# Optimization experiments

Hardware: AMD Instinct MI355X
Metric: run time of the kernel (lower is better)

Reference implementation:

```python
import jax, jax.numpy as jnp
import numpy as np

EPS = 1e-5  # BatchNorm eps
N_NODES, N_EDGES, F = 100000, 600000, 128


def setup_inputs() -> dict:
    key = jax.random.key(0)
    ks = jax.random.split(key, 16)
    inp = {
        "node_representations": jax.random.normal(ks[0], (N_NODES, F), jnp.float32),
        "edges": jax.random.randint(ks[1], (2, N_EDGES), 0, N_NODES, jnp.int64 if jax.config.jax_enable_x64 else jnp.int32),
        "edge_weights": jax.random.uniform(ks[2], (N_EDGES,), jnp.float32),
        # preprocess FFN: BatchNorm1d(F) [eval mode] + Linear(F, F) + GELU
        "pre_bn_gamma": jax.random.normal(ks[3], (F,), jnp.float32) * 0.1 + 1.0,
        "pre_bn_beta": jax.random.normal(ks[4], (F,), jnp.float32) * 0.1,
        "pre_bn_mean": jax.random.normal(ks[5], (F,), jnp.float32) * 0.1,
        "pre_bn_var": jax.random.uniform(ks[6], (F,), jnp.float32) * 0.5 + 0.5,
        "pre_w": jax.random.normal(ks[7], (F, F), jnp.float32) / np.sqrt(F),
        "pre_b": jnp.zeros((F,), jnp.float32),
        # update FFN: BatchNorm1d(2F) [eval mode] + Linear(2F, F) + GELU
        "upd_bn_gamma": jax.random.normal(ks[8], (2 * F,), jnp.float32) * 0.1 + 1.0,
        "upd_bn_beta": jax.random.normal(ks[9], (2 * F,), jnp.float32) * 0.1,
        "upd_bn_mean": jax.random.normal(ks[10], (2 * F,), jnp.float32) * 0.1,
        "upd_bn_var": jax.random.uniform(ks[11], (2 * F,), jnp.float32) * 0.5 + 0.5,
        "upd_w": jax.random.normal(ks[12], (2 * F, F), jnp.float32) / np.sqrt(2 * F),
        "upd_b": jnp.zeros((F,), jnp.float32),
    }
    return inp


def _bn_eval(x, gamma, beta, mean, var):
    return (x - mean) * (gamma / jnp.sqrt(var + EPS)) + beta


def reference(node_representations, edges, edge_weights,
              pre_bn_gamma, pre_bn_beta, pre_bn_mean, pre_bn_var, pre_w, pre_b,
              upd_bn_gamma, upd_bn_beta, upd_bn_mean, upd_bn_var, upd_w, upd_b):
    n_nodes, f = node_representations.shape
    node_idx, nbr_idx = edges[0], edges[1]
    # gather neighbour features: [E, F]
    x = node_representations[nbr_idx]
    # preprocess FFN (BN eval, dropout=identity in eval, linear, gelu)
    x = _bn_eval(x, pre_bn_gamma, pre_bn_beta, pre_bn_mean, pre_bn_var)
    x = jax.nn.gelu(x @ pre_w + pre_b, approximate=False)
    x = x * edge_weights[:, None]
    # mean aggregation (replicates torch.unique-on-expanded-indices counter = degree * F)
    agg = jax.ops.segment_sum(x, node_idx, num_segments=n_nodes)
    deg = jax.ops.segment_sum(jnp.ones_like(edge_weights), node_idx, num_segments=n_nodes)
    counter = (deg * f)[:, None]
    agg = jnp.where(counter > 0, agg / jnp.where(counter > 0, counter, 1.0), 0.0)
    # concat combine + update FFN
    emb = jnp.concatenate([node_representations, agg], axis=-1)
    emb = _bn_eval(emb, upd_bn_gamma, upd_bn_beta, upd_bn_mean, upd_bn_var)
    emb = jax.nn.gelu(emb @ upd_w + upd_b, approximate=False)
    return emb
```

## Files before the change

### kernel.cpp

```cpp
#include <hip/hip_runtime.h>
#include <math.h>

#define F 128
#define TWO_F 256
#define BN_EPS 1e-5f
#define PAD_W1 136
#define PAD_W2 264

typedef unsigned short ushort_t;
typedef unsigned char uchar_t;
typedef __attribute__((ext_vector_type(8))) short bfrag;
typedef __attribute__((ext_vector_type(4))) float ffrag;
typedef __attribute__((ext_vector_type(2))) float floatx2;

__device__ __forceinline__ float gelu_exact(float x) {
    return 0.5f * x * (1.0f + erff(x * 0.70710678118654752f));
}
__device__ __forceinline__ ushort_t f2bf(float x) {
    unsigned int u = __float_as_uint(x);
    u = (u + 0x7FFFu + ((u >> 16) & 1u)) >> 16;
    return (ushort_t)u;
}
__device__ __forceinline__ unsigned int pk2(float a, float b) {
    return (unsigned int)f2bf(a) | ((unsigned int)f2bf(b) << 16);
}

__device__ __forceinline__ void fma4_fp8(float* acc, unsigned int d, float w) {
    floatx2 lo = __builtin_amdgcn_cvt_pk_f32_fp8(d, false);
    floatx2 hi = __builtin_amdgcn_cvt_pk_f32_fp8(d, true);
    acc[0] = fmaf(w, lo.x, acc[0]);
    acc[1] = fmaf(w, lo.y, acc[1]);
    acc[2] = fmaf(w, hi.x, acc[2]);
    acc[3] = fmaf(w, hi.y, acc[3]);
}
__device__ __forceinline__ void fma16_fp8(float* acc, uint4 a, float w) {
    fma4_fp8(acc + 0,  a.x, w); fma4_fp8(acc + 4,  a.y, w);
    fma4_fp8(acc + 8,  a.z, w); fma4_fp8(acc + 12, a.w, w);
}

__device__ __forceinline__ bfrag pack8(float4 f0, float4 f1) {
    bfrag a;
    unsigned int* au = reinterpret_cast<unsigned int*>(&a);
    au[0] = pk2(f0.x, f0.y); au[1] = pk2(f0.z, f0.w);
    au[2] = pk2(f1.x, f1.y); au[3] = pk2(f1.z, f1.w);
    return a;
}

__global__ __launch_bounds__(256) void fold_hist(
    const float* __restrict__ pre_w, const float* __restrict__ pre_b,
    const float* __restrict__ g1, const float* __restrict__ be1,
    const float* __restrict__ m1, const float* __restrict__ v1,
    const float* __restrict__ upd_w, const float* __restrict__ upd_b,
    const float* __restrict__ g2, const float* __restrict__ be2,
    const float* __restrict__ m2, const float* __restrict__ v2,
    ushort_t* __restrict__ W1T, ushort_t* __restrict__ W2T,
    float* __restrict__ b1f, float* __restrict__ b2f,
    const int* __restrict__ edges, int* __restrict__ counts,
    int* __restrict__ rankb, int nEdges, int histBlocks) {
    const int t = threadIdx.x;
    if (blockIdx.x == 0) {
        __shared__ float t1[F], t2[TWO_F];
        if (t < F) {
            float s = g1[t] * rsqrtf(v1[t] + BN_EPS);
            t1[t] = be1[t] - m1[t] * s;
        }
        {
            float s = g2[t] * rsqrtf(v2[t] + BN_EPS);
            t2[t] = be2[t] - m2[t] * s;
        }
        __syncthreads();
        if (t < F) {
            float acc = pre_b[t];
            #pragma unroll 16
            for (int k = 0; k < F; ++k) acc = fmaf(t1[k], pre_w[k * F + t], acc);
            b1f[t] = acc;
        } else {
            int j = t - F;
            float acc = upd_b[j];
            #pragma unroll 16
            for (int k = 0; k < TWO_F; ++k) acc = fmaf(t2[k], upd_w[k * F + j], acc);
            b2f[j] = acc;
        }
    } else if (blockIdx.x <= 128) {
        int idx = (blockIdx.x - 1) * 256 + t;
        if (idx < F * F) {
            int k = idx & (F - 1), n = idx >> 7;
            float s = g1[k] * rsqrtf(v1[k] + BN_EPS);
            W1T[idx] = f2bf(s * pre_w[k * F + n]);
        }
        {
            int k = idx & (TWO_F - 1), n = idx >> 8;
            float s = g2[k] * rsqrtf(v2[k] + BN_EPS);
            W2T[idx] = f2bf(s * upd_w[k * F + n]);
        }
    } else {
        int b = blockIdx.x - 129;
        for (int i = b * 256 + t; i < nEdges; i += histBlocks * 256) {
            int rk = atomicAdd(&counts[edges[i]], 1);
            rankb[i] = rk;
        }
    }
}

__global__ __launch_bounds__(1024) void scan_pass1(const int* __restrict__ counts,
                                                   int* __restrict__ offsets,
                                                   int* __restrict__ blocksums, int n) {
    __shared__ int sb[1024];
    const int t = threadIdx.x;
    int idx = blockIdx.x * 1024 + t;
    int v = (idx < n) ? counts[idx] : 0;
    sb[t] = v;
    __syncthreads();
    for (int off = 1; off < 1024; off <<= 1) {
        int x = (t >= off) ? sb[t - off] : 0;
        __syncthreads();
        sb[t] += x;
        __syncthreads();
    }
    if (idx < n) offsets[idx + 1] = sb[t];
    if (t == 1023) blocksums[blockIdx.x] = sb[t];
}

__global__ __launch_bounds__(1024) void scan_pass3(const int* __restrict__ counts,
                                                   int* __restrict__ offsets,
                                                   const int* __restrict__ blocksums,
                                                   int* __restrict__ cursor, int n) {
    __shared__ int sb[1024];
    const int t = threadIdx.x;
    sb[t] = (t < blockIdx.x) ? blocksums[t] : 0;
    __syncthreads();
    #pragma unroll
    for (int off = 512; off > 0; off >>= 1) {
        if (t < off) sb[t] += sb[t + off];
        __syncthreads();
    }
    int base = sb[0];
    int idx = blockIdx.x * 1024 + t;
    if (idx < n) {
        int incl = offsets[idx + 1] + base;
        offsets[idx + 1] = incl;
        cursor[idx] = incl - counts[idx];
    }
    if (blockIdx.x == 0 && t == 0) offsets[0] = 0;
}

__global__ __launch_bounds__(256) void gemm1_fill(
    const float* __restrict__ nodes, const ushort_t* __restrict__ W1T,
    const float* __restrict__ b1f, uchar_t* __restrict__ G8, int nNodes,
    const int* __restrict__ edges, const float* __restrict__ ew,
    const int* __restrict__ offsets, const int* __restrict__ rankb,
    int2* __restrict__ csr, int nEdges, int gemmBlocks, int fillBlocks, int nTiles) {
    __shared__ ushort_t Wl[F * PAD_W1];
    __shared__ float bsm[F];
    const int t = threadIdx.x;

    if (blockIdx.x >= gemmBlocks) {
        int b = blockIdx.x - gemmBlocks;
        for (int e = b * 256 + t; e < nEdges; e += fillBlocks * 256) {
            int dst = edges[e];
            int pos = offsets[dst] + rankb[e];
            csr[pos] = make_int2(edges[nEdges + e], __float_as_int(ew[e]));
        }
        return;
    }

    for (int j = t; j < 2048; j += 256) {
        int feat = j >> 4, kc = j & 15;
        *reinterpret_cast<uint4*>(Wl + feat * PAD_W1 + kc * 8) =
            reinterpret_cast<const uint4*>(W1T)[j];
    }
    if (t < F) bsm[t] = b1f[t];
    __syncthreads();

    const int lane = t & 63, w = t >> 6;
    const int m = lane & 15, quad = lane >> 4;

    for (int tile = blockIdx.x; tile < nTiles; tile += gemmBlocks) {
        const int node = tile * 64 + w * 16 + m;
        const int sn = (node < nNodes) ? node : 0;
        const float* np = nodes + (size_t)sn * F + quad * 8;

        bfrag nf[4];
        #pragma unroll
        for (int kk = 0; kk < 4; ++kk) {
            float4 f0 = *reinterpret_cast<const float4*>(np + kk * 32);
            float4 f1 = *reinterpret_cast<const float4*>(np + kk * 32 + 4);
            nf[kk] = pack8(f0, f1);
        }

        ffrag acc[8];
        #pragma unroll
        for (int cb = 0; cb < 8; ++cb) acc[cb] = (ffrag){0.f, 0.f, 0.f, 0.f};

        #pragma unroll
        for (int kk = 0; kk < 4; ++kk) {
            int ko = kk * 32 + quad * 8;
            #pragma unroll
            for (int cb = 0; cb < 8; ++cb) {
                bfrag a = *reinterpret_cast<const bfrag*>(Wl + (cb * 16 + m) * PAD_W1 + ko);
                acc[cb] = __builtin_amdgcn_mfma_f32_16x16x32_bf16(a, nf[kk], acc[cb], 0, 0, 0);
            }
        }

        if (node < nNodes) {
            #pragma unroll
            for (int cb = 0; cb < 8; ++cb) {
                float4 bj = *reinterpret_cast<const float4*>(bsm + cb * 16 + quad * 4);
                float v0 = gelu_exact(acc[cb][0] + bj.x);
                float v1 = gelu_exact(acc[cb][1] + bj.y);
                float v2 = gelu_exact(acc[cb][2] + bj.z);
                float v3 = gelu_exact(acc[cb][3] + bj.w);
                int pw = __builtin_amdgcn_cvt_pk_fp8_f32(v0, v1, 0, false);
                pw = __builtin_amdgcn_cvt_pk_fp8_f32(v2, v3, pw, true);
                *reinterpret_cast<unsigned int*>(
                    G8 + (size_t)node * F + cb * 16 + quad * 4) = (unsigned int)pw;
            }
        }
    }
}

__global__ __launch_bounds__(256) void gather_agg(
    const uchar_t* __restrict__ G8, const int* __restrict__ offsets,
    const int2* __restrict__ csr, ushort_t* __restrict__ agg, int nNodes) {
    const int t = threadIdx.x;
    const int gid = blockIdx.x * 32 + (t >> 3);
    const int q = t & 7;
    if (gid >= nNodes) return;
    const int s = offsets[gid], e = offsets[gid + 1];

    float acc[16];
    #pragma unroll
    for (int j = 0; j < 16; ++j) acc[j] = 0.f;

    int i = s;
    while (i < e) {
        int c = e - i;
        c = (c > 8) ? 8 : c;
        uint4 av[8];
        float wv[8];
        #pragma unroll
        for (int j = 0; j < 8; ++j) {
            if (j < c) {
                int2 m = csr[i + j];
                wv[j] = __int_as_float(m.y);
                av[j] = *reinterpret_cast<const uint4*>(
                    G8 + (size_t)(unsigned int)m.x * F + q * 16);
            }
        }
        #pragma unroll
        for (int j = 0; j < 8; ++j)
            if (j < c) fma16_fp8(acc, av[j], wv[j]);
        i += c;
    }

    const int deg = e - s;
    const float inv = (deg > 0) ? 1.0f / ((float)deg * (float)F) : 0.f;
    uint4 pv0, pv1;
    pv0.x = pk2(acc[0] * inv, acc[1] * inv);  pv0.y = pk2(acc[2] * inv, acc[3] * inv);
    pv0.z = pk2(acc[4] * inv, acc[5] * inv);  pv0.w = pk2(acc[6] * inv, acc[7] * inv);
    pv1.x = pk2(acc[8] * inv, acc[9] * inv);  pv1.y = pk2(acc[10] * inv, acc[11] * inv);
    pv1.z = pk2(acc[12] * inv, acc[13] * inv); pv1.w = pk2(acc[14] * inv, acc[15] * inv);
    uint4* d = reinterpret_cast<uint4*>(agg + (size_t)gid * F + q * 16);
    d[0] = pv0; d[1] = pv1;
}

__global__ __launch_bounds__(512) void gemm2(
    const float* __restrict__ nodes, const ushort_t* __restrict__ agg,
    const ushort_t* __restrict__ W2T, const float* __restrict__ b2f,
    float* __restrict__ out, int nNodes) {
    __shared__ ushort_t Wl[F * PAD_W2];
    __shared__ float bsm[F];
    const int t = threadIdx.x;

    for (int j = t; j < 4096; j += 512) {
        int feat = j >> 5, kc = j & 31;
        *reinterpret_cast<uint4*>(Wl + feat * PAD_W2 + kc * 8) =
            reinterpret_cast<const uint4*>(W2T)[j];
    }
    if (t < F) bsm[t] = b2f[t];
    __syncthreads();

    const int lane = t & 63, w = t >> 6;
    const int m = lane & 15, quad = lane >> 4;

    const int node = blockIdx.x * 128 + w * 16 + m;
    const int sn = (node < nNodes) ? node : 0;
    const float*    np = nodes + (size_t)sn * F + quad * 8;
    const ushort_t* pa = agg   + (size_t)sn * F + quad * 8;

    bfrag nf[8];
    #pragma unroll
    for (int kk = 0; kk < 4; ++kk) {
        float4 f0 = *reinterpret_cast<const float4*>(np + kk * 32);
        float4 f1 = *reinterpret_cast<const float4*>(np + kk * 32 + 4);
        nf[kk] = pack8(f0, f1);
    }
    #pragma unroll
    for (int kk = 4; kk < 8; ++kk)
        nf[kk] = *reinterpret_cast<const bfrag*>(pa + (kk - 4) * 32);

    ffrag acc[8];
    #pragma unroll
    for (int cb = 0; cb < 8; ++cb) acc[cb] = (ffrag){0.f, 0.f, 0.f, 0.f};

    #pragma unroll
    for (int kk = 0; kk < 8; ++kk) {
        int ko = kk * 32 + quad * 8;
        #pragma unroll
        for (int cb = 0; cb < 8; ++cb) {
            bfrag a = *reinterpret_cast<const bfrag*>(Wl + (cb * 16 + m) * PAD_W2 + ko);
            acc[cb] = __builtin_amdgcn_mfma_f32_16x16x32_bf16(a, nf[kk], acc[cb], 0, 0, 0);
        }
    }

    if (node < nNodes) {
        #pragma unroll
        for (int cb = 0; cb < 8; ++cb) {
            float4 bj = *reinterpret_cast<const float4*>(bsm + cb * 16 + quad * 4);
            float4 o;
            o.x = gelu_exact(acc[cb][0] + bj.x);
            o.y = gelu_exact(acc[cb][1] + bj.y);
            o.z = gelu_exact(acc[cb][2] + bj.z);
            o.w = gelu_exact(acc[cb][3] + bj.w);
            *reinterpret_cast<float4*>(out + (size_t)node * F + cb * 16 + quad * 4) = o;
        }
    }
}

extern "C" void kernel_launch(void* const* d_in, const int* in_sizes, int n_in,
                              void* d_out, int out_size, void* d_ws, size_t ws_size,
                              hipStream_t stream) {
    const float* nodes  = (const float*)d_in[0];
    const int*   edges  = (const int*)d_in[1];
    const float* ew     = (const float*)d_in[2];
    const float* pre_g  = (const float*)d_in[3];
    const float* pre_be = (const float*)d_in[4];
    const float* pre_m  = (const float*)d_in[5];
    const float* pre_v  = (const float*)d_in[6];
    const float* pre_w  = (const float*)d_in[7];
    const float* pre_b  = (const float*)d_in[8];
    const float* upd_g  = (const float*)d_in[9];
    const float* upd_be = (const float*)d_in[10];
    const float* upd_m  = (const float*)d_in[11];
    const float* upd_v  = (const float*)d_in[12];
    const float* upd_w  = (const float*)d_in[13];
    const float* upd_b  = (const float*)d_in[14];
    float* out = (float*)d_out;

    const int nNodes = in_sizes[0] / F;
    const int nEdges = in_sizes[2];
    const int nChunks = (nNodes + 1023) / 1024;
    const int histBlocks = 1024;
    const int fillBlocks = 512;
    const int nTiles = (nNodes + 63) / 64;
    const int gemmBlocks = (nTiles < 1024) ? nTiles : 1024;

    char* p = (char*)d_ws;
    int*      counts    = (int*)p;       p += (size_t)nNodes * 4;
    int*      offsets   = (int*)p;       p += (size_t)(nNodes + 4) * 4;
    int*      cursor    = (int*)p;       p += (size_t)nNodes * 4;
    int*      blocksums = (int*)p;       p += 1024 * 4;
    int2*     csr       = (int2*)p;      p += (size_t)nEdges * 8;
    float*    b1f       = (float*)p;     p += F * 4;
    float*    b2f       = (float*)p;     p += F * 4;
    ushort_t* W1T       = (ushort_t*)p;  p += F * F * 2;
    ushort_t* W2T       = (ushort_t*)p;  p += TWO_F * F * 2;
    uchar_t*  G8        = (uchar_t*)p;   p += (size_t)nNodes * F;
    ushort_t* agg       = (ushort_t*)p;  p += (size_t)nNodes * F * 2;
    int*      rankb     = (int*)p;

    hipMemsetAsync(counts, 0, (size_t)nNodes * 4, stream);

    fold_hist<<<129 + histBlocks, 256, 0, stream>>>(
        pre_w, pre_b, pre_g, pre_be, pre_m, pre_v,
        upd_w, upd_b, upd_g, upd_be, upd_m, upd_v,
        W1T, W2T, b1f, b2f, edges, counts, rankb, nEdges, histBlocks);

    scan_pass1<<<nChunks, 1024, 0, stream>>>(counts, offsets, blocksums, nNodes);
    scan_pass3<<<nChunks, 1024, 0, stream>>>(counts, offsets, blocksums, cursor, nNodes);

    gemm1_fill<<<gemmBlocks + fillBlocks, 256, 0, stream>>>(
        nodes, W1T, b1f, G8, nNodes, edges, ew, offsets, rankb, csr, nEdges,
        gemmBlocks, fillBlocks, nTiles);

    gather_agg<<<(nNodes + 31) / 32, 256, 0, stream>>>(
        G8, offsets, csr, agg, nNodes);

    gemm2<<<(nNodes + 127) / 128, 512, 0, stream>>>(
        nodes, agg, W2T, b2f, out, nNodes);
}
```

Measured before the change: 250.3 us.

## Approximate GELU erf with polynomial and reorder weight LDS into fragment layout

Replaces the library erff in exact GELU with an Abramowitz-Stegun style polynomial and fast exp, making the activation epilogue cheaper in both GEMM kernels. It also rearranges the shared-memory weight tiles into an MFMA-fragment-contiguous order rather than padded rows, so each lane's fragment read is a linear 16-byte access with no bank conflicts and less padding. The erf approximation has an absolute error around 1e-7, which may be acceptable within tolerance but is no longer the exact erf.

```diff
diff --git a/kernel.cpp b/kernel.cpp
--- a/kernel.cpp
+++ b/kernel.cpp
@@ -4,8 +4,6 @@
 #define F 128
 #define TWO_F 256
 #define BN_EPS 1e-5f
-#define PAD_W1 136
-#define PAD_W2 264
 
 typedef unsigned short ushort_t;
 typedef unsigned char uchar_t;
@@ -14,7 +12,14 @@
 typedef __attribute__((ext_vector_type(2))) float floatx2;
 
 __device__ __forceinline__ float gelu_exact(float x) {
-    return 0.5f * x * (1.0f + erff(x * 0.70710678118654752f));
+    float a = fabsf(x) * 0.70710678118654752f;
+    float t = __fdividef(1.0f, fmaf(0.3275911f, a, 1.0f));
+    float poly = fmaf(fmaf(fmaf(fmaf(1.061405429f, t, -1.453152027f),
+                               t, 1.421413741f), t, -0.284496736f), t, 0.254829592f) * t;
+    float e = __expf(-a * a);
+    float erf_a = fmaf(-poly, e, 1.0f);
+    float erf_y = copysignf(erf_a, x);
+    return 0.5f * x * (1.0f + erf_y);
 }
 __device__ __forceinline__ ushort_t f2bf(float x) {
     unsigned int u = __float_as_uint(x);
@@ -150,7 +155,7 @@
     const int* __restrict__ edges, const float* __restrict__ ew,
     const int* __restrict__ offsets, const int* __restrict__ rankb,
     int2* __restrict__ csr, int nEdges, int gemmBlocks, int fillBlocks, int nTiles) {
-    __shared__ ushort_t Wl[F * PAD_W1];
+    __shared__ ushort_t Wl[16384];
     __shared__ float bsm[F];
     const int t = threadIdx.x;
 
@@ -164,10 +169,11 @@
         return;
     }
 
-    for (int j = t; j < 2048; j += 256) {
-        int feat = j >> 4, kc = j & 15;
-        *reinterpret_cast<uint4*>(Wl + feat * PAD_W1 + kc * 8) =
-            reinterpret_cast<const uint4*>(W1T)[j];
+    for (int c = t; c < 2048; c += 256) {
+        int m_ = c & 15, quad_ = (c >> 4) & 3, kk_ = (c >> 6) & 3, cb_ = c >> 8;
+        int feat = cb_ * 16 + m_;
+        *reinterpret_cast<uint4*>(Wl + (size_t)c * 8) =
+            *reinterpret_cast<const uint4*>(W1T + (size_t)feat * F + kk_ * 32 + quad_ * 8);
     }
     if (t < F) bsm[t] = b1f[t];
     __syncthreads();
@@ -194,10 +200,10 @@
 
         #pragma unroll
         for (int kk = 0; kk < 4; ++kk) {
-            int ko = kk * 32 + quad * 8;
             #pragma unroll
             for (int cb = 0; cb < 8; ++cb) {
-                bfrag a = *reinterpret_cast<const bfrag*>(Wl + (cb * 16 + m) * PAD_W1 + ko);
+                bfrag a = *reinterpret_cast<const bfrag*>(
+                    Wl + (size_t)((((cb * 4 + kk) * 4 + quad) * 16 + m) * 8));
                 acc[cb] = __builtin_amdgcn_mfma_f32_16x16x32_bf16(a, nf[kk], acc[cb], 0, 0, 0);
             }
         }
@@ -268,14 +274,15 @@
     const float* __restrict__ nodes, const ushort_t* __restrict__ agg,
     const ushort_t* __restrict__ W2T, const float* __restrict__ b2f,
     float* __restrict__ out, int nNodes) {
-    __shared__ ushort_t Wl[F * PAD_W2];
+    __shared__ ushort_t Wl[32768];
     __shared__ float bsm[F];
     const int t = threadIdx.x;
 
-    for (int j = t; j < 4096; j += 512) {
-        int feat = j >> 5, kc = j & 31;
-        *reinterpret_cast<uint4*>(Wl + feat * PAD_W2 + kc * 8) =
-            reinterpret_cast<const uint4*>(W2T)[j];
+    for (int c = t; c < 4096; c += 512) {
+        int m_ = c & 15, quad_ = (c >> 4) & 3, kk_ = (c >> 6) & 7, cb_ = c >> 9;
+        int feat = cb_ * 16 + m_;
+        *reinterpret_cast<uint4*>(Wl + (size_t)c * 8) =
+            *reinterpret_cast<const uint4*>(W2T + (size_t)feat * TWO_F + kk_ * 32 + quad_ * 8);
     }
     if (t < F) bsm[t] = b2f[t];
     __syncthreads();
@@ -305,10 +312,10 @@
 
     #pragma unroll
     for (int kk = 0; kk < 8; ++kk) {
-        int ko = kk * 32 + quad * 8;
         #pragma unroll
         for (int cb = 0; cb < 8; ++cb) {
-            bfrag a = *reinterpret_cast<const bfrag*>(Wl + (cb * 16 + m) * PAD_W2 + ko);
+            bfrag a = *reinterpret_cast<const bfrag*>(
+                Wl + (size_t)((((cb * 8 + kk) * 4 + quad) * 16 + m) * 8));
             acc[cb] = __builtin_amdgcn_mfma_f32_16x16x32_bf16(a, nf[kk], acc[cb], 0, 0, 0);
         }
     }
```

Result: faster. 245.2 us (-2.0%).
